# Optimization experiments

Hardware: AMD Instinct MI355X
Metric: run time of the kernel (lower is better)

Reference implementation:

```python
import jax, jax.numpy as jnp
import numpy as np

NH = 8          # number of attention heads
RAND_P = 0.1    # random attention probability
EPS = 1e-5      # LayerNorm eps (torch default)


def _layer_norm(x, g, b):
    m = x.mean(-1, keepdims=True)
    v = ((x - m) ** 2).mean(-1, keepdims=True)
    return (x - m) * jax.lax.rsqrt(v + EPS) * g + b


def _make_mask(u, n_frames, spatial):
    # random(0/1) + tiled-eye position mask + block-diagonal frame mask (additive float mask)
    L = n_frames * spatial
    idx = jnp.arange(L)
    frame_id = idx // spatial
    pos_id = idx % spatial
    rand = (u >= RAND_P).astype(jnp.float32)
    pos = (pos_id[:, None] == pos_id[None, :]).astype(jnp.float32)
    frame = (frame_id[:, None] == frame_id[None, :]).astype(jnp.float32)
    return rand + pos + frame  # [L, L], values in {0,1,2,3}


def _attn_block(f, u, Wqkv, bqkv, Wo, bo, g1, b1, Wfc1, bfc1, Wfc2, bfc2, g2, b2):
    N, C, H, W = f.shape
    S = H * W
    L = N * S
    hd = C // NH
    src = f.transpose(0, 2, 3, 1).reshape(L, C)  # (n,h,w) flatten order, batch=1 squeezed
    mask = _make_mask(u, N, S)

    qkv = src @ Wqkv.T + bqkv                    # [L, 3C]
    q, k, v = jnp.split(qkv, 3, axis=-1)
    q = q.reshape(L, NH, hd).transpose(1, 0, 2) * (hd ** -0.5)  # [H, L, hd]
    k = k.reshape(L, NH, hd).transpose(1, 0, 2)
    v = v.reshape(L, NH, hd).transpose(1, 0, 2)

    scores = jnp.einsum('hqd,hkd->hqk', q, k) + mask[None]      # [H, L, L]
    attn = jax.nn.softmax(scores, axis=-1)
    o = jnp.einsum('hqk,hkd->hqd', attn, v).transpose(1, 0, 2).reshape(L, C)
    src2 = o @ Wo.T + bo

    x = _layer_norm(src + src2, g1, b1)          # residual + LN (dropout p=0 -> identity)
    h = jax.nn.relu(x @ Wfc1.T + bfc1)
    x = _layer_norm(x + h @ Wfc2.T + bfc2, g2, b2)
    return x.reshape(N, H, W, C).transpose(0, 3, 1, 2)


def setup_inputs() -> dict:
    key = jax.random.key(0)
    ks = jax.random.split(key, 12)
    D = 256
    s = 0.02
    return {
        'f0': jax.random.normal(ks[0], (2, D, 80, 80), jnp.float32),
        'f1': jax.random.normal(ks[1], (2, D, 40, 40), jnp.float32),
        'f2': jax.random.normal(ks[2], (2, D, 32, 32), jnp.float32),
        'f3': jax.random.normal(ks[3], (2, D, 16, 16), jnp.float32),
        'u2': jax.random.uniform(ks[4], (2048, 2048), jnp.float32),
        'u3': jax.random.uniform(ks[5], (512, 512), jnp.float32),
        'Wqkv': jax.random.normal(ks[6], (3 * D, D), jnp.float32) * s,
        'bqkv': jnp.zeros((3 * D,), jnp.float32),
        'Wo': jax.random.normal(ks[7], (D, D), jnp.float32) * s,
        'bo': jnp.zeros((D,), jnp.float32),
        'g1': jnp.ones((D,), jnp.float32),
        'b1': jnp.zeros((D,), jnp.float32),
        'Wfc1': jax.random.normal(ks[8], (4 * D, D), jnp.float32) * s,
        'bfc1': jnp.zeros((4 * D,), jnp.float32),
        'Wfc2': jax.random.normal(ks[9], (D, 4 * D), jnp.float32) * s,
        'bfc2': jnp.zeros((D,), jnp.float32),
        'g2': jnp.ones((D,), jnp.float32),
        'b2': jnp.zeros((D,), jnp.float32),
    }


def reference(f0, f1, f2, f3, u2, u3, Wqkv, bqkv, Wo, bo, g1, b1,
              Wfc1, bfc1, Wfc2, bfc2, g2, b2):
    params = (Wqkv, bqkv, Wo, bo, g1, b1, Wfc1, bfc1, Wfc2, bfc2, g2, b2)
    # levels 0 and 1 pass through untouched (loop starts at i=2)
    out2 = _attn_block(f2, u2, *params)
    out3 = _attn_block(f3, u3, *params)
    return (f0, f1, out2, out3)
```

## Files before the change

### kernel.cpp

```cpp
#include <hip/hip_runtime.h>
#include <hip/hip_bf16.h>
#include <cstddef>


typedef __attribute__((ext_vector_type(8))) short s16x8;
typedef __attribute__((ext_vector_type(4))) short s16x4;
typedef __attribute__((ext_vector_type(4))) float f32x4;
typedef __attribute__((ext_vector_type(2))) unsigned int u32x2;
typedef unsigned short ushort_t;
typedef unsigned long long u64;

#define RTOT 2560
#define HIPL 69632

__device__ inline unsigned short f2bf(float x) {
    union { __hip_bfloat16 h; unsigned short u; } cv;
    cv.h = __float2bfloat16(x);
    return cv.u;
}
__device__ inline float bf2f(unsigned short u) {
    union { unsigned int i; float f; } cv;
    cv.i = ((unsigned int)u) << 16;
    return cv.f;
}

__global__ __launch_bounds__(256) void prep(const float* __restrict__ f0,
                                            const float* __restrict__ f1,
                                            float* __restrict__ outp,
                                            const float* __restrict__ wqkv,
                                            const float* __restrict__ wo,
                                            const float* __restrict__ wfc1,
                                            const float* __restrict__ wfc2,
                                            ushort_t* __restrict__ o1,
                                            ushort_t* __restrict__ o2,
                                            ushort_t* __restrict__ o3,
                                            ushort_t* __restrict__ o4,
                                            const float* __restrict__ u2,
                                            const float* __restrict__ u3,
                                            u64* __restrict__ ub,
                                            const float* __restrict__ f2,
                                            const float* __restrict__ f3,
                                            ushort_t* __restrict__ srcb) {
    __shared__ float tl[64][65];
    int bid = blockIdx.x;
    int t = threadIdx.x;
    if (bid < 160) {
        int b = bid;
        const float* src; int S, rowb, n, ct, ht;
        if (b < 128) {
            n = b >> 6; int rem = b & 63; ct = rem >> 4; ht = rem & 15;
            src = f2; S = 1024; rowb = 0;
        } else {
            int b2 = b - 128;
            n = b2 >> 4; int rem = b2 & 15; ct = rem >> 2; ht = rem & 3;
            src = f3; S = 256; rowb = 2048;
        }
        int c0 = ct * 64, hw0 = ht * 64;
        int i = t >> 6, lane = t & 63;
#pragma unroll
        for (int jj = 0; jj < 16; ++jj) {
            int cl = i * 16 + jj;
            tl[lane][cl] = src[(size_t)(n * 256 + c0 + cl) * S + hw0 + lane];
        }
        __syncthreads();
#pragma unroll
        for (int jj = 0; jj < 16; ++jj) {
            int hl = i * 16 + jj;
            int row = rowb + n * S + hw0 + hl;
            srcb[(size_t)row * 256 + c0 + lane] = f2bf(tl[hl][lane]);
        }
    } else if (bid < 4160) {
        int idx = (bid - 160) * 256 + t;
        f32x4 v = (idx < 819200) ? ((const f32x4*)f0)[idx]
                                 : ((const f32x4*)f1)[idx - 819200];
        ((f32x4*)outp)[idx] = v;
    } else if (bid < 4928) {
        int i = (bid - 4160) * 256 + t;
        const float* src; ushort_t* dst; int li;
        if (i < 49152)       { src = wqkv; dst = o1; li = i; }
        else if (i < 65536)  { src = wo;   dst = o2; li = i - 49152; }
        else if (i < 131072) { src = wfc1; dst = o3; li = i - 65536; }
        else                 { src = wfc2; dst = o4; li = i - 131072; }
        f32x4 v = ((const f32x4*)src)[li];
        s16x4 r;
        r[0] = (short)f2bf(v[0]); r[1] = (short)f2bf(v[1]);
        r[2] = (short)f2bf(v[2]); r[3] = (short)f2bf(v[3]);
        ((s16x4*)dst)[li] = r;
    } else {
        int gw = ((bid - 4928) * 256 + t) >> 6;
        int lane = t & 63;
        const float* p;
        u64* dstLo;
        int q, kb, smask, sshift;
        if (gw < 16384) {
            int row = gw >> 3, ch = gw & 7;
            p = &u2[(size_t)row * 2048 + ch * 256 + lane * 4];
            dstLo = &ub[(size_t)gw * 4];
            q = row; kb = ch * 256 + lane * 4; smask = 1023; sshift = 10;
        } else {
            int lw = gw - 16384;
            int row = lw >> 1, ch = lw & 1;
            p = &u3[(size_t)row * 512 + ch * 256 + lane * 4];
            dstLo = &ub[65536 + (size_t)lw * 4];
            q = row; kb = ch * 256 + lane * 4; smask = 255; sshift = 8;
        }
        u64* dstHi = dstLo + HIPL;
        f32x4 v = *(const f32x4*)p;
        int qp = q & smask, qf = q >> sshift;
        u64 bl[4], bh[4];
#pragma unroll
        for (int j = 0; j < 4; ++j) {
            int k = kb + j;
            int val = (v[j] >= 0.1f ? 1 : 0)
                    + ((k & smask) == qp ? 1 : 0)
                    + ((k >> sshift) == qf ? 1 : 0);
            bl[j] = __ballot((val & 1) != 0);
            bh[j] = __ballot((val & 2) != 0);
        }
        if (lane < 4) {
            u64 x = (lane == 0) ? bl[0] : (lane == 1) ? bl[1]
                  : (lane == 2) ? bl[2] : bl[3];
            dstLo[lane] = x;
        } else if (lane < 8) {
            int j = lane - 4;
            u64 x = (j == 0) ? bh[0] : (j == 1) ? bh[1]
                  : (j == 2) ? bh[2] : bh[3];
            dstHi[j] = x;
        }
    }
}

#define ASTR 72

template <int EPI>
__global__ __launch_bounds__(256) void gemm64(const ushort_t* __restrict__ A,
                                              const ushort_t* __restrict__ W,
                                              const float* __restrict__ bias,
                                              ushort_t* __restrict__ outb,
                                              int M, int N, int K) {
    __shared__ __align__(16) ushort_t As[2][64 * ASTR];
    __shared__ __align__(16) ushort_t Ws[2][64 * ASTR];

    const int t = threadIdx.x;
    const int w = t >> 6, l = t & 63;
    const int c = l & 15, g = l >> 4;
    const int mh = w >> 1, nh = w & 1;
    const int m0 = blockIdx.y * 64, n0 = blockIdx.x * 64;
    const int srow = t >> 3;
    const int cg8 = (t & 7) * 8;

    const ushort_t* Aip0 = &A[(size_t)(m0 + srow) * K + cg8];
    const ushort_t* Aip1 = &A[(size_t)(m0 + 32 + srow) * K + cg8];
    const ushort_t* Wip0 = &W[(size_t)(n0 + srow) * K + cg8];
    const ushort_t* Wip1 = &W[(size_t)(n0 + 32 + srow) * K + cg8];

    s16x8 ra0 = *(const s16x8*)Aip0;
    s16x8 ra1 = *(const s16x8*)Aip1;
    s16x8 rw0 = *(const s16x8*)Wip0;
    s16x8 rw1 = *(const s16x8*)Wip1;
    *(s16x8*)&As[0][srow * ASTR + cg8] = ra0;
    *(s16x8*)&As[0][(32 + srow) * ASTR + cg8] = ra1;
    *(s16x8*)&Ws[0][srow * ASTR + cg8] = rw0;
    *(s16x8*)&Ws[0][(32 + srow) * ASTR + cg8] = rw1;
    __syncthreads();

    f32x4 acc[2][2] = {{{0.f,0.f,0.f,0.f},{0.f,0.f,0.f,0.f}},
                       {{0.f,0.f,0.f,0.f},{0.f,0.f,0.f,0.f}}};
    const int nsteps = K >> 6;

    for (int ks = 0; ks < nsteps; ++ks) {
        const int b = ks & 1;
        const bool pf = (ks + 1 < nsteps);
        if (pf) {
            int ko = (ks + 1) << 6;
            ra0 = *(const s16x8*)(Aip0 + ko);
            ra1 = *(const s16x8*)(Aip1 + ko);
            rw0 = *(const s16x8*)(Wip0 + ko);
            rw1 = *(const s16x8*)(Wip1 + ko);
        }
#pragma unroll
        for (int sl = 0; sl < 2; ++sl) {
            s16x8 af0 = *(const s16x8*)&As[b][(32 * mh + c) * ASTR + sl * 32 + 8 * g];
            s16x8 af1 = *(const s16x8*)&As[b][(32 * mh + 16 + c) * ASTR + sl * 32 + 8 * g];
            s16x8 wf0 = *(const s16x8*)&Ws[b][(32 * nh + c) * ASTR + sl * 32 + 8 * g];
            s16x8 wf1 = *(const s16x8*)&Ws[b][(32 * nh + 16 + c) * ASTR + sl * 32 + 8 * g];
            acc[0][0] = __builtin_amdgcn_mfma_f32_16x16x32_bf16(af0, wf0, acc[0][0], 0, 0, 0);
            acc[0][1] = __builtin_amdgcn_mfma_f32_16x16x32_bf16(af0, wf1, acc[0][1], 0, 0, 0);
            acc[1][0] = __builtin_amdgcn_mfma_f32_16x16x32_bf16(af1, wf0, acc[1][0], 0, 0, 0);
            acc[1][1] = __builtin_amdgcn_mfma_f32_16x16x32_bf16(af1, wf1, acc[1][1], 0, 0, 0);
        }
        if (pf) {
            int nb = b ^ 1;
            *(s16x8*)&As[nb][srow * ASTR + cg8] = ra0;
            *(s16x8*)&As[nb][(32 + srow) * ASTR + cg8] = ra1;
            *(s16x8*)&Ws[nb][srow * ASTR + cg8] = rw0;
            *(s16x8*)&Ws[nb][(32 + srow) * ASTR + cg8] = rw1;
        }
        __syncthreads();
    }

#pragma unroll
    for (int i = 0; i < 2; ++i)
#pragma unroll
    for (int j = 0; j < 2; ++j) {
        int n = n0 + 32 * nh + 16 * j + c;
        float bv = bias[n];
        float sc = 1.f;
        if (EPI == 3) sc = (n < 256) ? 0.17677669529663687f : 1.f;
#pragma unroll
        for (int r = 0; r < 4; ++r) {
            int m = m0 + 32 * mh + 16 * i + 4 * g + r;
            float v = acc[i][j][r] + bv;
            if (EPI == 1) v = fmaxf(v, 0.f);
            if (EPI == 3) v *= sc;
            outb[(size_t)m * N + n] = f2bf(v);
        }
    }
}

__global__ __launch_bounds__(128) void gemm_fc2(const ushort_t* __restrict__ A,
                                                const ushort_t* __restrict__ W,
                                                const float* __restrict__ bias,
                                                const ushort_t* __restrict__ res,
                                                ushort_t* __restrict__ outb,
                                                int M, int N, int K) {
    __shared__ __align__(16) ushort_t As[2][32 * ASTR];
    __shared__ __align__(16) ushort_t Ws[2][32 * ASTR];

    const int t = threadIdx.x;
    const int w = t >> 6, l = t & 63;
    const int c = l & 15, g = l >> 4;
    const int m0 = blockIdx.y * 32, n0 = blockIdx.x * 32;
    const int srow = t >> 3;
    const int cg8 = (t & 7) * 8;

    const ushort_t* Aip0 = &A[(size_t)(m0 + srow) * K + cg8];
    const ushort_t* Aip1 = &A[(size_t)(m0 + 16 + srow) * K + cg8];
    const ushort_t* Wip0 = &W[(size_t)(n0 + srow) * K + cg8];
    const ushort_t* Wip1 = &W[(size_t)(n0 + 16 + srow) * K + cg8];

    s16x8 ra0 = *(const s16x8*)Aip0;
    s16x8 ra1 = *(const s16x8*)Aip1;
    s16x8 rw0 = *(const s16x8*)Wip0;
    s16x8 rw1 = *(const s16x8*)Wip1;
    *(s16x8*)&As[0][srow * ASTR + cg8] = ra0;
    *(s16x8*)&As[0][(16 + srow) * ASTR + cg8] = ra1;
    *(s16x8*)&Ws[0][srow * ASTR + cg8] = rw0;
    *(s16x8*)&Ws[0][(16 + srow) * ASTR + cg8] = rw1;
    __syncthreads();

    f32x4 acc[2] = {{0.f, 0.f, 0.f, 0.f}, {0.f, 0.f, 0.f, 0.f}};
    const int nsteps = K >> 6;

    for (int ks = 0; ks < nsteps; ++ks) {
        const int b = ks & 1;
        const bool pf = (ks + 1 < nsteps);
        if (pf) {
            int ko = (ks + 1) << 6;
            ra0 = *(const s16x8*)(Aip0 + ko);
            ra1 = *(const s16x8*)(Aip1 + ko);
            rw0 = *(const s16x8*)(Wip0 + ko);
            rw1 = *(const s16x8*)(Wip1 + ko);
        }
#pragma unroll
        for (int kt = 0; kt < 2; ++kt) {
            s16x8 af = *(const s16x8*)&As[b][(16 * w + c) * ASTR + kt * 32 + 8 * g];
            s16x8 wf0 = *(const s16x8*)&Ws[b][c * ASTR + kt * 32 + 8 * g];
            s16x8 wf1 = *(const s16x8*)&Ws[b][(16 + c) * ASTR + kt * 32 + 8 * g];
            acc[0] = __builtin_amdgcn_mfma_f32_16x16x32_bf16(af, wf0, acc[0], 0, 0, 0);
            acc[1] = __builtin_amdgcn_mfma_f32_16x16x32_bf16(af, wf1, acc[1], 0, 0, 0);
        }
        if (pf) {
            int nb = b ^ 1;
            *(s16x8*)&As[nb][srow * ASTR + cg8] = ra0;
            *(s16x8*)&As[nb][(16 + srow) * ASTR + cg8] = ra1;
            *(s16x8*)&Ws[nb][srow * ASTR + cg8] = rw0;
            *(s16x8*)&Ws[nb][(16 + srow) * ASTR + cg8] = rw1;
        }
        __syncthreads();
    }

#pragma unroll
    for (int nt = 0; nt < 2; ++nt) {
        int n = n0 + 16 * nt + c;
        float bv = bias[n];
#pragma unroll
        for (int r = 0; r < 4; ++r) {
            int m = m0 + 16 * w + 4 * g + r;
            float v = acc[nt][r] + bv + bf2f(res[(size_t)m * N + n]);
            outb[(size_t)m * N + n] = f2bf(v);
        }
    }
}

__global__ __launch_bounds__(128) void gemm_wo(const ushort_t* __restrict__ Opart,
                                               const float2* __restrict__ ml,
                                               const ushort_t* __restrict__ W,
                                               const float* __restrict__ bias,
                                               const ushort_t* __restrict__ res,
                                               ushort_t* __restrict__ outb) {
    const int K = 256, N = 256;
    __shared__ __align__(16) ushort_t As[2][32 * ASTR];
    __shared__ __align__(16) ushort_t Ws[2][32 * ASTR];

    const int t = threadIdx.x;
    const int w = t >> 6, l = t & 63;
    const int c = l & 15, g = l >> 4;
    const int m0 = blockIdx.y * 32, n0 = blockIdx.x * 32;
    const int srow = t >> 3;
    const int cg8 = (t & 7) * 8;

    auto loadA = [&](int row, int kcol) -> s16x8 {
        int head = kcol >> 5;
        float2 a0 = ml[((size_t)0 * RTOT + row) * 8 + head];
        float2 a1 = ml[((size_t)1 * RTOT + row) * 8 + head];
        float2 a2 = ml[((size_t)2 * RTOT + row) * 8 + head];
        float2 a3 = ml[((size_t)3 * RTOT + row) * 8 + head];
        float M = fmaxf(fmaxf(a0.x, a1.x), fmaxf(a2.x, a3.x));
        float w1 = __expf(a0.x - M), w2 = __expf(a1.x - M);
        float w3 = __expf(a2.x - M), w4 = __expf(a3.x - M);
        float inv = 1.f / (w1 * a0.y + w2 * a1.y + w3 * a2.y + w4 * a3.y);
        const size_t str = (size_t)RTOT * 256;
        size_t base = (size_t)row * 256 + kcol;
        s16x8 o1 = *(const s16x8*)&Opart[base];
        s16x8 o2 = *(const s16x8*)&Opart[base + str];
        s16x8 o3 = *(const s16x8*)&Opart[base + 2 * str];
        s16x8 o4 = *(const s16x8*)&Opart[base + 3 * str];
        s16x8 r;
#pragma unroll
        for (int e = 0; e < 8; ++e) {
            float v = w1 * bf2f((ushort_t)o1[e]) + w2 * bf2f((ushort_t)o2[e])
                    + w3 * bf2f((ushort_t)o3[e]) + w4 * bf2f((ushort_t)o4[e]);
            r[e] = (short)f2bf(v * inv);
        }
        return r;
    };

    const ushort_t* Wip0 = &W[(size_t)(n0 + srow) * K + cg8];
    const ushort_t* Wip1 = &W[(size_t)(n0 + 16 + srow) * K + cg8];

    s16x8 ra0 = loadA(m0 + srow, cg8);
    s16x8 ra1 = loadA(m0 + 16 + srow, cg8);
    s16x8 rw0 = *(const s16x8*)Wip0;
    s16x8 rw1 = *(const s16x8*)Wip1;
    *(s16x8*)&As[0][srow * ASTR + cg8] = ra0;
    *(s16x8*)&As[0][(16 + srow) * ASTR + cg8] = ra1;
    *(s16x8*)&Ws[0][srow * ASTR + cg8] = rw0;
    *(s16x8*)&Ws[0][(16 + srow) * ASTR + cg8] = rw1;
    __syncthreads();

    f32x4 acc[2] = {{0.f, 0.f, 0.f, 0.f}, {0.f, 0.f, 0.f, 0.f}};
    const int nsteps = 4;

    for (int ks = 0; ks < nsteps; ++ks) {
        const int b = ks & 1;
        const bool pf = (ks + 1 < nsteps);
        if (pf) {
            int ko = (ks + 1) << 6;
            ra0 = loadA(m0 + srow, ko + cg8);
            ra1 = loadA(m0 + 16 + srow, ko + cg8);
            rw0 = *(const s16x8*)(Wip0 + ko);
            rw1 = *(const s16x8*)(Wip1 + ko);
        }
#pragma unroll
        for (int kt = 0; kt < 2; ++kt) {
            s16x8 af = *(const s16x8*)&As[b][(16 * w + c) * ASTR + kt * 32 + 8 * g];
            s16x8 wf0 = *(const s16x8*)&Ws[b][c * ASTR + kt * 32 + 8 * g];
            s16x8 wf1 = *(const s16x8*)&Ws[b][(16 + c) * ASTR + kt * 32 + 8 * g];
            acc[0] = __builtin_amdgcn_mfma_f32_16x16x32_bf16(af, wf0, acc[0], 0, 0, 0);
            acc[1] = __builtin_amdgcn_mfma_f32_16x16x32_bf16(af, wf1, acc[1], 0, 0, 0);
        }
        if (pf) {
            int nb = b ^ 1;
            *(s16x8*)&As[nb][srow * ASTR + cg8] = ra0;
            *(s16x8*)&As[nb][(16 + srow) * ASTR + cg8] = ra1;
            *(s16x8*)&Ws[nb][srow * ASTR + cg8] = rw0;
            *(s16x8*)&Ws[nb][(16 + srow) * ASTR + cg8] = rw1;
        }
        __syncthreads();
    }

#pragma unroll
    for (int nt = 0; nt < 2; ++nt) {
        int n = n0 + 16 * nt + c;
        float bv = bias[n];
#pragma unroll
        for (int r = 0; r < 4; ++r) {
            int m = m0 + 16 * w + 4 * g + r;
            float v = acc[nt][r] + bv + bf2f(res[(size_t)m * 256 + n]);
            outb[(size_t)m * 256 + n] = f2bf(v);
        }
    }
}

#define KS 40
#define VS 66
#define PS 72
#define OS 68

__global__ __launch_bounds__(256) void flash_split(const ushort_t* __restrict__ qkvb,
                                                   const u64* __restrict__ ubits,
                                                   ushort_t* __restrict__ Opart,
                                                   float2* __restrict__ ml) {
    __shared__ __align__(16) ushort_t ks[2][64 * KS];
    __shared__ __align__(16) ushort_t vts[2][32 * VS];
    __shared__ __align__(16) char pso[64 * PS * 2];
    ushort_t* ps = (ushort_t*)pso;
    float* os = (float*)pso;

    const int bx = blockIdx.x;
    int qt, h, split, L, rowbase;
    const u64* ub;
    if (bx < 1024) {
        qt = bx & 31; h = (bx >> 5) & 7; split = bx >> 8;
        L = 2048; rowbase = 0; ub = ubits;
    } else {
        int lo = bx - 1024;
        qt = lo & 7; h = (lo >> 3) & 7; split = lo >> 6;
        L = 512; rowbase = 2048; ub = ubits + 65536;
    }
    const int tps = (L >> 6) >> 2;
    const int ts0 = split * tps;
    const int nch = L >> 8;

    const int t = threadIdx.x;
    const int w = t >> 6;
    const int l = t & 63;
    const int c = l & 15;
    const int g = l >> 4;

    const int srow = t >> 2;
    const int sc8 = (t & 3) * 8;
    const int q0g = rowbase + qt * 64;

    const int ql = qt * 64 + 16 * w + c;
    const s16x8 qf = *(const s16x8*)&qkvb[(size_t)(rowbase + ql) * 768 + h * 32 + 8 * g];
    const u64* ubq = &ub[(size_t)ql * nch * 4];

    s16x8 kreg, vreg;
    {
        size_t base = (size_t)(rowbase + ts0 * 64 + srow) * 768 + h * 32 + sc8;
        s16x8 k0r = *(const s16x8*)&qkvb[base + 256];
        s16x8 v0r = *(const s16x8*)&qkvb[base + 512];
        *(s16x8*)&ks[0][srow * KS + sc8] = k0r;
#pragma unroll
        for (int i = 0; i < 8; ++i)
            vts[0][(sc8 + i) * VS + srow] = (ushort_t)v0r[i];
        if (tps > 1) {
            kreg = *(const s16x8*)&qkvb[base + 64 * 768 + 256];
            vreg = *(const s16x8*)&qkvb[base + 64 * 768 + 512];
        }
    }
    __syncthreads();

    f32x4 oacc0 = {0.f, 0.f, 0.f, 0.f};
    f32x4 oacc1 = {0.f, 0.f, 0.f, 0.f};
    float mold = -3e38f;
    float lsum = 0.f;
    const f32x4 zc = {0.f, 0.f, 0.f, 0.f};

    u64 wl0 = 0, wl1 = 0, wl2 = 0, wl3 = 0;
    u64 wh0 = 0, wh1 = 0, wh2 = 0, wh3 = 0;
    int cur = 0;
    for (int kt = 0; kt < tps; ++kt) {
        const int nxt = cur ^ 1;
        const int gt = ts0 + kt;

        if (kt + 1 < tps) {
            *(s16x8*)&ks[nxt][srow * KS + sc8] = kreg;
#pragma unroll
            for (int i = 0; i < 8; ++i)
                vts[nxt][(sc8 + i) * VS + srow] = (ushort_t)vreg[i];
        }
        if (kt + 2 < tps) {
            size_t base = (size_t)(rowbase + (gt + 2) * 64 + srow) * 768 + h * 32 + sc8;
            kreg = *(const s16x8*)&qkvb[base + 256];
            vreg = *(const s16x8*)&qkvb[base + 512];
        }

        if ((gt & 3) == 0 || kt == 0) {
            const u64* bp = &ubq[(size_t)(gt >> 2) * 4];
            wl0 = bp[0]; wl1 = bp[1]; wl2 = bp[2]; wl3 = bp[3];
            wh0 = bp[HIPL]; wh1 = bp[HIPL + 1]; wh2 = bp[HIPL + 2]; wh3 = bp[HIPL + 3];
        }
        const unsigned shb = 16 * (gt & 3);

        f32x4 sacc[4];
        __builtin_amdgcn_s_setprio(1);
#pragma unroll
        for (int nt = 0; nt < 4; ++nt) {
            s16x8 kf = *(const s16x8*)&ks[cur][(16 * nt + c) * KS + 8 * g];
            sacc[nt] = __builtin_amdgcn_mfma_f32_16x16x32_bf16(kf, qf, zc, 0, 0, 0);
        }
        __builtin_amdgcn_s_setprio(0);

        float sv[4][4];
        float pmax = -3e38f;
#pragma unroll
        for (int nt = 0; nt < 4; ++nt) {
            unsigned sh = shb + 4 * nt + g;
#pragma unroll
            for (int r = 0; r < 4; ++r) {
                u64 wl = (r == 0) ? wl0 : (r == 1) ? wl1 : (r == 2) ? wl2 : wl3;
                u64 wh = (r == 0) ? wh0 : (r == 1) ? wh1 : (r == 2) ? wh2 : wh3;
                unsigned lo = (unsigned)(wl >> sh) & 1u;
                unsigned hi = (unsigned)(wh >> sh) & 1u;
                float s = sacc[nt][r] + (float)(lo + 2u * hi);
                sv[nt][r] = s;
                pmax = fmaxf(pmax, s);
            }
        }
        if (!__all(pmax <= mold + 8.f)) {
            float m = pmax;
            m = fmaxf(m, __shfl_xor(m, 16));
            m = fmaxf(m, __shfl_xor(m, 32));
            float newm = fmaxf(mold, m);
            float fac = __expf(mold - newm);
            mold = newm;
            lsum *= fac;
            oacc0 *= fac;
            oacc1 *= fac;
        }

        float sum = 0.f;
#pragma unroll
        for (int nt = 0; nt < 4; ++nt) {
            float p0 = __expf(sv[nt][0] - mold);
            float p1 = __expf(sv[nt][1] - mold);
            float p2 = __expf(sv[nt][2] - mold);
            float p3 = __expf(sv[nt][3] - mold);
            sum += (p0 + p1) + (p2 + p3);
            u32x2 pk;
            pk[0] = ((unsigned)f2bf(p1) << 16) | f2bf(p0);
            pk[1] = ((unsigned)f2bf(p3) << 16) | f2bf(p2);
            *(u32x2*)&ps[(16 * w + c) * PS + 16 * nt + 4 * g] = pk;
        }
        lsum += sum;

        __builtin_amdgcn_s_setprio(1);
#pragma unroll
        for (int kc = 0; kc < 2; ++kc) {
            s16x8 pfr = *(const s16x8*)&ps[(16 * w + c) * PS + 32 * kc + 8 * g];
            s16x8 vf0 = *(const s16x8*)&vts[cur][c * VS + 32 * kc + 8 * g];
            s16x8 vf1 = *(const s16x8*)&vts[cur][(16 + c) * VS + 32 * kc + 8 * g];
            oacc0 = __builtin_amdgcn_mfma_f32_16x16x32_bf16(vf0, pfr, oacc0, 0, 0, 0);
            oacc1 = __builtin_amdgcn_mfma_f32_16x16x32_bf16(vf1, pfr, oacc1, 0, 0, 0);
        }
        __builtin_amdgcn_s_setprio(0);

        __syncthreads();
        cur = nxt;
    }

    float lrun = lsum;
    lrun += __shfl_xor(lrun, 16);
    lrun += __shfl_xor(lrun, 32);

    if (g == 0) {
        int q = q0g + 16 * w + c;
        ml[((size_t)split * RTOT + q) * 8 + h] = make_float2(mold, lrun);
    }

#pragma unroll
    for (int r = 0; r < 4; ++r) {
        os[(4 * g + r) * OS + 16 * w + c] = oacc0[r];
        os[(16 + 4 * g + r) * OS + 16 * w + c] = oacc1[r];
    }
    __syncthreads();
    {
        int r = t >> 2, d0 = (t & 3) * 8;
        s16x8 pk;
#pragma unroll
        for (int i = 0; i < 8; ++i) pk[i] = (short)f2bf(os[(d0 + i) * OS + r]);
        *(s16x8*)&Opart[((size_t)split * RTOT + q0g + r) * 256 + h * 32 + d0] = pk;
    }
}

__global__ __launch_bounds__(256) void ln1_kernel(const ushort_t* __restrict__ in,
                                                  const float* __restrict__ g,
                                                  const float* __restrict__ b,
                                                  ushort_t* __restrict__ outb) {
    __shared__ float red[256];
    int row = blockIdx.x, t = threadIdx.x;
    size_t idx = (size_t)row * 256 + t;
    float v = bf2f(in[idx]);
    red[t] = v;
    __syncthreads();
    for (int s = 128; s > 0; s >>= 1) {
        if (t < s) red[t] += red[t + s];
        __syncthreads();
    }
    float mean = red[0] * (1.f / 256.f);
    __syncthreads();
    float d = v - mean;
    red[t] = d * d;
    __syncthreads();
    for (int s = 128; s > 0; s >>= 1) {
        if (t < s) red[t] += red[t + s];
        __syncthreads();
    }
    float var = red[0] * (1.f / 256.f);
    float r = d * rsqrtf(var + 1e-5f) * g[t] + b[t];
    outb[idx] = f2bf(r);
}

__global__ __launch_bounds__(256) void ln2_out(const ushort_t* __restrict__ in,
                                               const float* __restrict__ g,
                                               const float* __restrict__ b,
                                               float* __restrict__ out2,
                                               float* __restrict__ out3) {
    __shared__ float red[256];
    int row = blockIdx.x, t = threadIdx.x;
    size_t idx = (size_t)row * 256 + t;
    float v = bf2f(in[idx]);
    red[t] = v;
    __syncthreads();
    for (int s = 128; s > 0; s >>= 1) {
        if (t < s) red[t] += red[t + s];
        __syncthreads();
    }
    float mean = red[0] * (1.f / 256.f);
    __syncthreads();
    float d = v - mean;
    red[t] = d * d;
    __syncthreads();
    for (int s = 128; s > 0; s >>= 1) {
        if (t < s) red[t] += red[t + s];
        __syncthreads();
    }
    float var = red[0] * (1.f / 256.f);
    float r = d * rsqrtf(var + 1e-5f) * g[t] + b[t];
    if (row < 2048) {
        int n = row >> 10, hw = row & 1023;
        out2[((size_t)(n * 256 + t) << 10) + hw] = r;
    } else {
        int rl = row - 2048;
        int n = rl >> 8, hw = rl & 255;
        out3[((size_t)(n * 256 + t) << 8) + hw] = r;
    }
}


extern "C" void kernel_launch(void* const* d_in, const int* in_sizes, int n_in,
                              void* d_out, int out_size, void* d_ws, size_t ws_size,
                              hipStream_t stream) {
    const float* f0 = (const float*)d_in[0];
    const float* f1 = (const float*)d_in[1];
    const float* f2 = (const float*)d_in[2];
    const float* f3 = (const float*)d_in[3];
    const float* u2 = (const float*)d_in[4];
    const float* u3 = (const float*)d_in[5];
    const float* Wqkv = (const float*)d_in[6];
    const float* bqkv = (const float*)d_in[7];
    const float* Wo   = (const float*)d_in[8];
    const float* bo   = (const float*)d_in[9];
    const float* g1   = (const float*)d_in[10];
    const float* b1   = (const float*)d_in[11];
    const float* Wfc1 = (const float*)d_in[12];
    const float* bfc1 = (const float*)d_in[13];
    const float* Wfc2 = (const float*)d_in[14];
    const float* bfc2 = (const float*)d_in[15];
    const float* g2   = (const float*)d_in[16];
    const float* b2   = (const float*)d_in[17];

    float* out = (float*)d_out;
    float* ws = (float*)d_ws;

    ushort_t* wqkv = (ushort_t*)ws;
    ushort_t* wo   = (ushort_t*)(ws + 98304);
    ushort_t* wfc1 = (ushort_t*)(ws + 131072);
    ushort_t* wfc2 = (ushort_t*)(ws + 262144);

    float* sc = ws + 393216;
    ushort_t* src_bf = (ushort_t*)sc;
    ushort_t* qkvb   = (ushort_t*)(sc + 327680);
    ushort_t* t1b    = (ushort_t*)(sc + 1310720);
    ushort_t* x_bf   = (ushort_t*)(sc + 1638400);
    ushort_t* t2b    = (ushort_t*)(sc + 1966080);
    u64*      ubits  = (u64*)(sc + 2293760);
    float2*   ml     = (float2*)(sc + 2572288);
    ushort_t* Opart  = (ushort_t*)(sc + 2736128);
    ushort_t* h_bf   = Opart;

    prep<<<9280, 256, 0, stream>>>(f0, f1, out,
                                   Wqkv, Wo, Wfc1, Wfc2, wqkv, wo, wfc1, wfc2,
                                   u2, u3, ubits, f2, f3, src_bf);

    gemm64<3><<<dim3(12, 40), 256, 0, stream>>>(
        src_bf, wqkv, bqkv, qkvb, RTOT, 768, 256);
    flash_split<<<1280, 256, 0, stream>>>(qkvb, ubits, Opart, ml);
    gemm_wo<<<dim3(8, 80), 128, 0, stream>>>(Opart, ml, wo, bo, src_bf, t1b);
    ln1_kernel<<<2560, 256, 0, stream>>>(t1b, g1, b1, x_bf);
    gemm64<1><<<dim3(16, 40), 256, 0, stream>>>(
        x_bf, wfc1, bfc1, h_bf, RTOT, 1024, 256);
    gemm_fc2<<<dim3(8, 80), 128, 0, stream>>>(
        h_bf, wfc2, bfc2, x_bf, t2b, RTOT, 256, 1024);
    ln2_out<<<2560, 256, 0, stream>>>(t2b, g2, b2, out + 4096000, out + 4620288);
}
```

Measured before the change: 86.35 us.

## Use exp2 softmax, wave-per-row LayerNorm, and tiled transpose for LN2 output

The Q scale and mask values are folded with log2(e) so flash attention and the merge step can use exp2 in place of exp. The rescale threshold is widened to match the base-2 scale. LN1 is rewritten to process one row per wavefront with 4-element vector loads and shuffle reductions instead of a shared-memory tree with many barriers. LN2 is split into a stats kernel and a scatter kernel that transposes 64x64 tiles through shared memory, so the NCHW output writes are coalesced. This adds one extra launch and uses a single-pass variance that is less numerically robust.

```diff
diff --git a/kernel.cpp b/kernel.cpp
--- a/kernel.cpp
+++ b/kernel.cpp
@@ -1,6 +1,7 @@
 #include <hip/hip_runtime.h>
 #include <hip/hip_bf16.h>
 #include <cstddef>
+#include <cmath>
 
 
 typedef __attribute__((ext_vector_type(8))) short s16x8;
@@ -12,6 +13,7 @@
 
 #define RTOT 2560
 #define HIPL 69632
+#define LOG2E 1.4426950408889634f
 
 __device__ inline unsigned short f2bf(float x) {
     union { __hip_bfloat16 h; unsigned short u; } cv;
@@ -23,6 +25,7 @@
     cv.i = ((unsigned int)u) << 16;
     return cv.f;
 }
+__device__ inline float fexp2(float x) { return exp2f(x); }
 
 __global__ __launch_bounds__(256) void prep(const float* __restrict__ f0,
                                             const float* __restrict__ f1,
@@ -206,7 +209,7 @@
         int n = n0 + 32 * nh + 16 * j + c;
         float bv = bias[n];
         float sc = 1.f;
-        if (EPI == 3) sc = (n < 256) ? 0.17677669529663687f : 1.f;
+        if (EPI == 3) sc = (n < 256) ? 0.17677669529663687f * LOG2E : 1.f;
 #pragma unroll
         for (int r = 0; r < 4; ++r) {
             int m = m0 + 32 * mh + 16 * i + 4 * g + r;
@@ -317,8 +320,8 @@
         float2 a2 = ml[((size_t)2 * RTOT + row) * 8 + head];
         float2 a3 = ml[((size_t)3 * RTOT + row) * 8 + head];
         float M = fmaxf(fmaxf(a0.x, a1.x), fmaxf(a2.x, a3.x));
-        float w1 = __expf(a0.x - M), w2 = __expf(a1.x - M);
-        float w3 = __expf(a2.x - M), w4 = __expf(a3.x - M);
+        float w1 = fexp2(a0.x - M), w2 = fexp2(a1.x - M);
+        float w3 = fexp2(a2.x - M), w4 = fexp2(a3.x - M);
         float inv = 1.f / (w1 * a0.y + w2 * a1.y + w3 * a2.y + w4 * a3.y);
         const size_t str = (size_t)RTOT * 256;
         size_t base = (size_t)row * 256 + kcol;
@@ -505,17 +508,17 @@
                 u64 wh = (r == 0) ? wh0 : (r == 1) ? wh1 : (r == 2) ? wh2 : wh3;
                 unsigned lo = (unsigned)(wl >> sh) & 1u;
                 unsigned hi = (unsigned)(wh >> sh) & 1u;
-                float s = sacc[nt][r] + (float)(lo + 2u * hi);
+                float s = fmaf((float)(lo + 2u * hi), LOG2E, sacc[nt][r]);
                 sv[nt][r] = s;
                 pmax = fmaxf(pmax, s);
             }
         }
-        if (!__all(pmax <= mold + 8.f)) {
+        if (!__all(pmax <= mold + 11.5415f)) {
             float m = pmax;
             m = fmaxf(m, __shfl_xor(m, 16));
             m = fmaxf(m, __shfl_xor(m, 32));
             float newm = fmaxf(mold, m);
-            float fac = __expf(mold - newm);
+            float fac = fexp2(mold - newm);
             mold = newm;
             lsum *= fac;
             oacc0 *= fac;
@@ -525,10 +528,10 @@
         float sum = 0.f;
 #pragma unroll
         for (int nt = 0; nt < 4; ++nt) {
-            float p0 = __expf(sv[nt][0] - mold);
-            float p1 = __expf(sv[nt][1] - mold);
-            float p2 = __expf(sv[nt][2] - mold);
-            float p3 = __expf(sv[nt][3] - mold);
+            float p0 = fexp2(sv[nt][0] - mold);
+            float p1 = fexp2(sv[nt][1] - mold);
+            float p2 = fexp2(sv[nt][2] - mold);
+            float p3 = fexp2(sv[nt][3] - mold);
             sum += (p0 + p1) + (p2 + p3);
             u32x2 pk;
             pk[0] = ((unsigned)f2bf(p1) << 16) | f2bf(p0);
@@ -580,63 +583,95 @@
                                                   const float* __restrict__ g,
                                                   const float* __restrict__ b,
                                                   ushort_t* __restrict__ outb) {
-    __shared__ float red[256];
-    int row = blockIdx.x, t = threadIdx.x;
-    size_t idx = (size_t)row * 256 + t;
-    float v = bf2f(in[idx]);
-    red[t] = v;
+    int t = threadIdx.x;
+    int row = blockIdx.x * 4 + (t >> 6);
+    int lane = t & 63;
+    size_t base = (size_t)row * 256 + lane * 4;
+    s16x4 x = *(const s16x4*)&in[base];
+    float v[4];
+    float s1 = 0.f, s2 = 0.f;
+#pragma unroll
+    for (int e = 0; e < 4; ++e) {
+        v[e] = bf2f((ushort_t)x[e]);
+        s1 += v[e];
+        s2 += v[e] * v[e];
+    }
+#pragma unroll
+    for (int d = 1; d < 64; d <<= 1) {
+        s1 += __shfl_xor(s1, d);
+        s2 += __shfl_xor(s2, d);
+    }
+    float mean = s1 * (1.f / 256.f);
+    float var = s2 * (1.f / 256.f) - mean * mean;
+    float rstd = rsqrtf(var + 1e-5f);
+    s16x4 r;
+#pragma unroll
+    for (int e = 0; e < 4; ++e) {
+        int n = lane * 4 + e;
+        r[e] = (short)f2bf((v[e] - mean) * rstd * g[n] + b[n]);
+    }
+    *(s16x4*)&outb[base] = r;
+}
+
+__global__ __launch_bounds__(256) void ln2_stats(const ushort_t* __restrict__ in,
+                                                 float2* __restrict__ stats) {
+    int t = threadIdx.x;
+    int row = blockIdx.x * 4 + (t >> 6);
+    int lane = t & 63;
+    s16x4 x = *(const s16x4*)&in[(size_t)row * 256 + lane * 4];
+    float s1 = 0.f, s2 = 0.f;
+#pragma unroll
+    for (int e = 0; e < 4; ++e) {
+        float v = bf2f((ushort_t)x[e]);
+        s1 += v;
+        s2 += v * v;
+    }
+#pragma unroll
+    for (int d = 1; d < 64; d <<= 1) {
+        s1 += __shfl_xor(s1, d);
+        s2 += __shfl_xor(s2, d);
+    }
+    if (lane == 0) {
+        float mean = s1 * (1.f / 256.f);
+        float var = s2 * (1.f / 256.f) - mean * mean;
+        stats[row] = make_float2(mean, rsqrtf(var + 1e-5f));
+    }
+}
+
+__global__ __launch_bounds__(256) void ln2_scatter(const ushort_t* __restrict__ in,
+                                                   const float2* __restrict__ stats,
+                                                   const float* __restrict__ g,
+                                                   const float* __restrict__ b,
+                                                   float* __restrict__ out2,
+                                                   float* __restrict__ out3) {
+    __shared__ float tl[64][65];
+    int bid = blockIdx.x;
+    int t = threadIdx.x;
+    float* dst; int S, rowb, n, ct, ht;
+    if (bid < 128) {
+        n = bid >> 6; int rem = bid & 63; ct = rem >> 4; ht = rem & 15;
+        dst = out2; S = 1024; rowb = 0;
+    } else {
+        int b2 = bid - 128;
+        n = b2 >> 4; int rem = b2 & 15; ct = rem >> 2; ht = rem & 3;
+        dst = out3; S = 256; rowb = 2048;
+    }
+    int c0 = ct * 64, hw0 = ht * 64;
+    int i = t >> 6, lane = t & 63;
+    float gv = g[c0 + lane], bv = b[c0 + lane];
+#pragma unroll
+    for (int jj = 0; jj < 16; ++jj) {
+        int hl = i * 16 + jj;
+        int row = rowb + n * S + hw0 + hl;
+        float2 st = stats[row];
+        float v = bf2f(in[(size_t)row * 256 + c0 + lane]);
+        tl[hl][lane] = (v - st.x) * st.y * gv + bv;
+    }
     __syncthreads();
-    for (int s = 128; s > 0; s >>= 1) {
-        if (t < s) red[t] += red[t + s];
-        __syncthreads();
-    }
-    float mean = red[0] * (1.f / 256.f);
-    __syncthreads();
-    float d = v - mean;
-    red[t] = d * d;
-    __syncthreads();
-    for (int s = 128; s > 0; s >>= 1) {
-        if (t < s) red[t] += red[t + s];
-        __syncthreads();
-    }
-    float var = red[0] * (1.f / 256.f);
-    float r = d * rsqrtf(var + 1e-5f) * g[t] + b[t];
-    outb[idx] = f2bf(r);
-}
-
-__global__ __launch_bounds__(256) void ln2_out(const ushort_t* __restrict__ in,
-                                               const float* __restrict__ g,
-                                               const float* __restrict__ b,
-                                               float* __restrict__ out2,
-                                               float* __restrict__ out3) {
-    __shared__ float red[256];
-    int row = blockIdx.x, t = threadIdx.x;
-    size_t idx = (size_t)row * 256 + t;
-    float v = bf2f(in[idx]);
-    red[t] = v;
-    __syncthreads();
-    for (int s = 128; s > 0; s >>= 1) {
-        if (t < s) red[t] += red[t + s];
-        __syncthreads();
-    }
-    float mean = red[0] * (1.f / 256.f);
-    __syncthreads();
-    float d = v - mean;
-    red[t] = d * d;
-    __syncthreads();
-    for (int s = 128; s > 0; s >>= 1) {
-        if (t < s) red[t] += red[t + s];
-        __syncthreads();
-    }
-    float var = red[0] * (1.f / 256.f);
-    float r = d * rsqrtf(var + 1e-5f) * g[t] + b[t];
-    if (row < 2048) {
-        int n = row >> 10, hw = row & 1023;
-        out2[((size_t)(n * 256 + t) << 10) + hw] = r;
-    } else {
-        int rl = row - 2048;
-        int n = rl >> 8, hw = rl & 255;
-        out3[((size_t)(n * 256 + t) << 8) + hw] = r;
+#pragma unroll
+    for (int jj = 0; jj < 16; ++jj) {
+        int cl = i * 16 + jj;
+        dst[(size_t)(n * 256 + c0 + cl) * S + hw0 + lane] = tl[lane][cl];
     }
 }
 
@@ -679,7 +714,8 @@
     ushort_t* t2b    = (ushort_t*)(sc + 1966080);
     u64*      ubits  = (u64*)(sc + 2293760);
     float2*   ml     = (float2*)(sc + 2572288);
-    ushort_t* Opart  = (ushort_t*)(sc + 2736128);
+    float2*   st2    = (float2*)(sc + 2736128);
+    ushort_t* Opart  = (ushort_t*)(sc + 2741248);
     ushort_t* h_bf   = Opart;
 
     prep<<<9280, 256, 0, stream>>>(f0, f1, out,
@@ -690,10 +726,12 @@
         src_bf, wqkv, bqkv, qkvb, RTOT, 768, 256);
     flash_split<<<1280, 256, 0, stream>>>(qkvb, ubits, Opart, ml);
     gemm_wo<<<dim3(8, 80), 128, 0, stream>>>(Opart, ml, wo, bo, src_bf, t1b);
-    ln1_kernel<<<2560, 256, 0, stream>>>(t1b, g1, b1, x_bf);
+    ln1_kernel<<<640, 256, 0, stream>>>(t1b, g1, b1, x_bf);
     gemm64<1><<<dim3(16, 40), 256, 0, stream>>>(
         x_bf, wfc1, bfc1, h_bf, RTOT, 1024, 256);
     gemm_fc2<<<dim3(8, 80), 128, 0, stream>>>(
         h_bf, wfc2, bfc2, x_bf, t2b, RTOT, 256, 1024);
-    ln2_out<<<2560, 256, 0, stream>>>(t2b, g2, b2, out + 4096000, out + 4620288);
-}
+    ln2_stats<<<640, 256, 0, stream>>>(t2b, st2);
+    ln2_scatter<<<160, 256, 0, stream>>>(t2b, st2, g2, b2,
+                                         out + 4096000, out + 4620288);
+}
```

Result: faster. 82.10 us (-4.9%).
